# Performance work log

Hardware: AMD Instinct MI355X
Metric: run time of the kernel (lower is better)

## Reference

```python
import jax, jax.numpy as jnp
import numpy as np

N_NODES = 100000
N_EDGES = 1600000
D_IN = 128
D_OUT = 128
KEEP_PROB = 0.5  # torch code: p_drop = 1 - self.dropout, dropout=0.5


def setup_inputs() -> dict:
    key = jax.random.key(0)
    k1, k2, k3, k4, k5 = jax.random.split(key, 5)
    x = jax.random.normal(k1, (N_NODES, D_IN), dtype=jnp.float32)
    # Glorot uniform init matching weight_variable_glorot
    init_range = np.sqrt(6.0 / (D_IN + D_OUT))
    W = jax.random.uniform(k2, (D_IN, D_OUT), dtype=jnp.float32,
                           minval=-init_range, maxval=init_range)
    adj_row = jax.random.randint(k3, (N_EDGES,), 0, N_NODES, dtype=jnp.int32)
    adj_col = jax.random.randint(k4, (N_EDGES,), 0, N_NODES, dtype=jnp.int32)
    adj_val = jax.random.uniform(k5, (N_EDGES,), dtype=jnp.float32)
    return {"x": x, "W": W, "adj_row": adj_row, "adj_col": adj_col, "adj_val": adj_val}


def reference(x, W, adj_row, adj_col, adj_val):
    # dropout (always training=True in the torch module), deterministic key
    mask = jax.random.bernoulli(jax.random.key(42), KEEP_PROB, x.shape)
    x = jnp.where(mask, x / KEEP_PROB, 0.0)
    # dense GEMM: [N, D_in] @ [D_in, D_out]
    h = x @ W
    # sparse adjacency SpMM in COO form: out[r] += val * h[c]
    msg = adj_val[:, None] * h[adj_col]            # [E, D_out]
    agg = jax.ops.segment_sum(msg, adj_row, num_segments=N_NODES)
    return jax.nn.relu(agg)
```

## Files before the change

### kernel.cpp

```cpp
#include <hip/hip_runtime.h>
#include <hip/hip_bf16.h>

#define N_NODES 100000
#define N_EDGES 1600000
#define D 128
#define NC 391
#define CCAP 5120
#define C1S 32
#define RSS 257
#define G2CAP 512

typedef float          floatx4 __attribute__((ext_vector_type(4)));
typedef __bf16         bf16x8  __attribute__((ext_vector_type(8)));
typedef unsigned short ushort8 __attribute__((ext_vector_type(8)));

__device__ __forceinline__ unsigned rotl32(unsigned x, int d) {
    return (x << d) | (x >> (32 - d));
}

__device__ __forceinline__ void threefry_0_42(unsigned c0, unsigned c1,
                                              unsigned& o0, unsigned& o1) {
    const unsigned k0 = 0u, k1 = 42u;
    const unsigned k2 = 0x1BD11BDAu ^ k0 ^ k1;
    unsigned x0 = c0 + k0;
    unsigned x1 = c1 + k1;
#define TF_R4(r0, r1, r2, r3)                      \
    x0 += x1; x1 = rotl32(x1, r0); x1 ^= x0;       \
    x0 += x1; x1 = rotl32(x1, r1); x1 ^= x0;       \
    x0 += x1; x1 = rotl32(x1, r2); x1 ^= x0;       \
    x0 += x1; x1 = rotl32(x1, r3); x1 ^= x0;
    TF_R4(13, 15, 26, 6);  x0 += k1; x1 += k2 + 1u;
    TF_R4(17, 29, 16, 24); x0 += k2; x1 += k0 + 2u;
    TF_R4(13, 15, 26, 6);  x0 += k0; x1 += k1 + 3u;
    TF_R4(17, 29, 16, 24); x0 += k1; x1 += k2 + 4u;
    TF_R4(13, 15, 26, 6);  x0 += k2; x1 += k0 + 5u;
#undef TF_R4
    o0 = x0; o1 = x1;
}

__device__ __forceinline__ bool keep_elem(unsigned i) {
    unsigned o0, o1;
    threefry_0_42(0u, i, o0, o1);
    return (((o0 ^ o1) >> 31) == 0u);
}

__device__ __forceinline__ unsigned short f32_bf16(float f) {
    unsigned u = __float_as_uint(f);
    u += 0x7fffu + ((u >> 16) & 1u);
    return (unsigned short)(u >> 16);
}

__global__ __launch_bounds__(256)
void k_wprep(const float* __restrict__ W, unsigned short* __restrict__ Wf,
             int* __restrict__ cnt1) {
    int g = blockIdx.x * 256 + threadIdx.x;
    for (int i = g; i < NC * C1S; i += 2048) cnt1[i] = 0;
    int combo = g >> 6, l = g & 63;
    int ct = combo >> 2, kt = combo & 3;
    int mm = l & 15, q = l >> 4;
    unsigned short tmp[8];
#pragma unroll
    for (int j = 0; j < 8; ++j)
        tmp[j] = f32_bf16(W[(kt * 32 + q * 8 + j) * 128 + ct * 16 + mm]);
    *(ushort8*)&Wf[g * 8] = *(ushort8*)tmp;
}

__global__ __launch_bounds__(256)
void k_bucket1(const int* __restrict__ row, const int* __restrict__ col,
               const float* __restrict__ val, int* __restrict__ cnt1,
               int2* __restrict__ buf) {
    __shared__ int h[NC];
    __shared__ int lbase[NC];
    const int t = threadIdx.x;
    for (int i = t; i < NC; i += 256) h[i] = 0;
    __syncthreads();

    int rows[16], cols[16];
    float vals[16];
    int base = blockIdx.x * 4096;
#pragma unroll
    for (int k = 0; k < 4; ++k) {
        int e4 = base + (k * 256 + t) * 4;
        if (e4 < N_EDGES) {
            *(int4*)&rows[k * 4]   = *(const int4*)(row + e4);
            *(int4*)&cols[k * 4]   = *(const int4*)(col + e4);
            *(float4*)&vals[k * 4] = *(const float4*)(val + e4);
        } else {
            rows[k * 4] = rows[k * 4 + 1] = rows[k * 4 + 2] = rows[k * 4 + 3] = -1;
        }
    }
#pragma unroll
    for (int j = 0; j < 16; ++j)
        if (rows[j] >= 0) atomicAdd(&h[rows[j] >> 8], 1);
    __syncthreads();

    for (int i = t; i < NC; i += 256) {
        int c = h[i];
        lbase[i] = c ? atomicAdd(&cnt1[i * C1S], c) : 0;
    }
    __syncthreads();
    for (int i = t; i < NC; i += 256) h[i] = 0;
    __syncthreads();

#pragma unroll
    for (int j = 0; j < 16; ++j) {
        if (rows[j] >= 0) {
            int bb  = rows[j] >> 8;
            int pos = lbase[bb] + atomicAdd(&h[bb], 1);
            if (pos < CCAP) {
                int2 ent;
                ent.x = (cols[j] << 7) | ((rows[j] & 255) << 24);
                ent.y = __float_as_int(vals[j]);
                buf[bb * CCAP + pos] = ent;
            }
        }
    }
}

__global__ __launch_bounds__(256)
void k_sort(const int* __restrict__ cnt1, int2* __restrict__ buf,
            int* __restrict__ rs) {
    __shared__ int h[4][256];
    __shared__ int wsum[4];

    const int t = threadIdx.x;
    const int c = blockIdx.x;
    const int w = t >> 6;
    int n = cnt1[c * C1S];
    if (n > CCAP) n = CCAP;
    int2* slab = buf + c * CCAP;

    for (int i = t; i < 1024; i += 256) ((int*)h)[i] = 0;
    __syncthreads();

    int2 er[20];
#pragma unroll
    for (int k = 0; k < 20; ++k) {
        int i = k * 256 + t;
        if (i < n) {
            er[k] = slab[i];
            atomicAdd(&h[w][((unsigned)er[k].x) >> 24], 1);
        }
    }
    __syncthreads();

    int v = h[0][t] + h[1][t] + h[2][t] + h[3][t];
    int xsc = v;
#pragma unroll
    for (int off = 1; off < 64; off <<= 1) {
        int u = __shfl_up(xsc, off);
        if ((t & 63) >= off) xsc += u;
    }
    if ((t & 63) == 63) wsum[t >> 6] = xsc;
    __syncthreads();
    int wo = 0;
    for (int k = 0; k < (t >> 6); ++k) wo += wsum[k];
    int basex = xsc - v + wo;
    rs[c * RSS + t] = basex;
    if (t == 0) rs[c * RSS + 256] = n;
    int s = basex;
#pragma unroll
    for (int wv = 0; wv < 4; ++wv) {
        int tmp = h[wv][t];
        h[wv][t] = s;
        s += tmp;
    }
    __syncthreads();

#pragma unroll
    for (int k = 0; k < 20; ++k) {
        int i = k * 256 + t;
        if (i < n) {
            int pos = atomicAdd(&h[w][((unsigned)er[k].x) >> 24], 1);
            slab[pos] = er[k];
        }
    }
}

__global__ __launch_bounds__(256)
void k_gemm(const float* __restrict__ x, const unsigned short* __restrict__ Wf,
            unsigned short* __restrict__ hb) {
    __shared__ __align__(16) unsigned short xs[32][136];
    const int t = threadIdx.x, g = blockIdx.x;

    {
        int m  = t >> 4;
        int c0 = (t & 15) * 8;
        int r0 = g * 32 + m;
        const float* pa = x + r0 * D + c0;
        const float* pb = x + (r0 + 16) * D + c0;
        float va[8], vb[8];
        *(float4*)&va[0] = ((const float4*)pa)[0];
        *(float4*)&va[4] = ((const float4*)pa)[1];
        *(float4*)&vb[0] = ((const float4*)pb)[0];
        *(float4*)&vb[4] = ((const float4*)pb)[1];
        int ibase = r0 * D + c0;
        unsigned short ta[8], tb[8];
#pragma unroll
        for (int j = 0; j < 8; ++j) {
            float fa = keep_elem((unsigned)(ibase + j))        ? 2.0f * va[j] : 0.0f;
            float fb = keep_elem((unsigned)(ibase + 2048 + j)) ? 2.0f * vb[j] : 0.0f;
            ta[j] = f32_bf16(fa);
            tb[j] = f32_bf16(fb);
        }
        *(ushort8*)&xs[m][c0]      = *(ushort8*)ta;
        *(ushort8*)&xs[16 + m][c0] = *(ushort8*)tb;
    }
    __syncthreads();

    const int w = t >> 6, l = t & 63;
    const int rt = w >> 1, ctbase = (w & 1) * 4;
    const int mm = l & 15, q = l >> 4, koff = q * 8;
    const unsigned short* xrow = &xs[rt * 16 + mm][0];
    bf16x8 af[4];
#pragma unroll
    for (int kt = 0; kt < 4; ++kt)
        af[kt] = *(const bf16x8*)(xrow + kt * 32 + koff);

    const int growbase = g * 32 + rt * 16;
#pragma unroll
    for (int ci = 0; ci < 4; ++ci) {
        int ct = ctbase + ci;
        bf16x8 wfc[4];
#pragma unroll
        for (int kt = 0; kt < 4; ++kt)
            wfc[kt] = *(const bf16x8*)&Wf[((ct * 4 + kt) * 64 + l) * 8];
        floatx4 acc = {0.f, 0.f, 0.f, 0.f};
#pragma unroll
        for (int kt = 0; kt < 4; ++kt)
            acc = __builtin_amdgcn_mfma_f32_16x16x32_bf16(af[kt], wfc[kt], acc, 0, 0, 0);
        int col = ct * 16 + mm;
#pragma unroll
        for (int reg = 0; reg < 4; ++reg) {
            int grow = growbase + q * 4 + reg;
            hb[grow * D + col] = f32_bf16(acc[reg]);
        }
    }
}

__global__ __launch_bounds__(256, 8)
void k_gather(const int* __restrict__ rs, const int2* __restrict__ buf,
              const unsigned short* __restrict__ hb, float* __restrict__ out) {
    __shared__ __align__(16) int2 eL[G2CAP];

    const int B = blockIdx.x, t = threadIdx.x;
    const int c = B >> 4;
    const int2* slab = buf + c * CCAP;
    const int* rsb = rs + c * RSS + (B & 15) * 16;
    const int rs0 = rsb[0];
    int nf = rsb[16] - rs0;
    if (nf > G2CAP) nf = G2CAP;

    for (int i = t; i < nf; i += 256) eL[i] = slab[rs0 + i];
    __syncthreads();

    const int w  = t >> 6;
    const int l2 = (t & 63) * 2;
    const unsigned short* hbl = hb + l2;
    for (int r = 0; r < 4; ++r) {
        int rl = w * 4 + r;
        int s0 = rsb[rl] - rs0;     if (s0 > nf) s0 = nf;
        int e0 = rsb[rl + 1] - rs0; if (e0 > nf) e0 = nf;
        int cc = e0 - s0;
        float a0 = 0.f, a1 = 0.f;
        int i = 0;
        for (; i + 16 <= cc; i += 16) {
            unsigned ex[16];
            float    vv[16];
#pragma unroll
            for (int j = 0; j < 16; ++j) {
                int2 e = eL[s0 + i + j];
                ex[j] = (unsigned)e.x & 0xFFFFFFu;
                vv[j] = __int_as_float(e.y);
            }
            unsigned hv[16];
#pragma unroll
            for (int j = 0; j < 16; ++j)
                hv[j] = *(const unsigned*)(hbl + ex[j]);
#pragma unroll
            for (int j = 0; j < 16; ++j) {
                a0 = fmaf(vv[j], __uint_as_float(hv[j] << 16), a0);
                a1 = fmaf(vv[j], __uint_as_float(hv[j] & 0xffff0000u), a1);
            }
        }
        for (; i + 4 <= cc; i += 4) {
            unsigned ex[4];
            float    vv[4];
#pragma unroll
            for (int j = 0; j < 4; ++j) {
                int2 e = eL[s0 + i + j];
                ex[j] = (unsigned)e.x & 0xFFFFFFu;
                vv[j] = __int_as_float(e.y);
            }
            unsigned hv[4];
#pragma unroll
            for (int j = 0; j < 4; ++j)
                hv[j] = *(const unsigned*)(hbl + ex[j]);
#pragma unroll
            for (int j = 0; j < 4; ++j) {
                a0 = fmaf(vv[j], __uint_as_float(hv[j] << 16), a0);
                a1 = fmaf(vv[j], __uint_as_float(hv[j] & 0xffff0000u), a1);
            }
        }
        for (; i < cc; ++i) {
            int2 e = eL[s0 + i];
            float v = __int_as_float(e.y);
            unsigned hv = *(const unsigned*)(hbl + ((unsigned)e.x & 0xFFFFFFu));
            a0 = fmaf(v, __uint_as_float(hv << 16), a0);
            a1 = fmaf(v, __uint_as_float(hv & 0xffff0000u), a1);
        }
        int grow = (B << 4) + rl;
        if (grow < N_NODES) {
            float2 rr;
            rr.x = a0 > 0.f ? a0 : 0.f;
            rr.y = a1 > 0.f ? a1 : 0.f;
            *(float2*)(out + grow * D + l2) = rr;
        }
    }
}

extern "C" void kernel_launch(void* const* d_in, const int* in_sizes, int n_in,
                              void* d_out, int out_size, void* d_ws, size_t ws_size,
                              hipStream_t stream) {
    const float* x    = (const float*)d_in[0];
    const float* W    = (const float*)d_in[1];
    const int*   arow = (const int*)d_in[2];
    const int*   acol = (const int*)d_in[3];
    const float* aval = (const float*)d_in[4];
    float* out = (float*)d_out;

    char* ws = (char*)d_ws;
    unsigned short* hb = (unsigned short*)ws;
    size_t off = 25600000;
    int* cnt1 = (int*)(ws + off); off += NC * C1S * 4;
    off = (off + 127) & ~(size_t)127;
    unsigned short* Wf = (unsigned short*)(ws + off); off += 32768;
    off = (off + 127) & ~(size_t)127;
    int* rs   = (int*)(ws + off); off += NC * RSS * 4;
    off = (off + 127) & ~(size_t)127;
    int2* buf = (int2*)(ws + off); off += (size_t)NC * CCAP * 8;

    k_wprep   <<<8, 256, 0, stream>>>(W, Wf, cnt1);
    k_bucket1 <<<NC, 256, 0, stream>>>(arow, acol, aval, cnt1, buf);
    k_sort    <<<NC, 256, 0, stream>>>(cnt1, buf, rs);
    k_gemm    <<<3125, 256, 0, stream>>>(x, Wf, hb);
    k_gather  <<<NC * 16, 256, 0, stream>>>(rs, buf, hb, out);
}
```

Baseline: 227.2 us.

## Widen bucketing grid, double sort block size, stage GEMM output through LDS

The bucketing kernel now handles 1024 edges per block across 1563 blocks instead of 4096 per block across 391, which spreads the scatter over more CUs. The sort kernel runs 512 threads with 8 per-wave histograms. Only the first 256 threads do the scan, and a split __syncthreads handles the branch. The GEMM epilogue writes bf16 results into the shared tile and then stores full 16-byte rows, replacing scattered 2-byte global writes. The trade-offs are more global atomics on cnt1 and the shared-buffer reuse, plus the divergent-barrier pattern in the sort.

```diff
diff --git a/kernel.cpp b/kernel.cpp
--- a/kernel.cpp
+++ b/kernel.cpp
@@ -9,6 +9,7 @@
 #define C1S 32
 #define RSS 257
 #define G2CAP 512
+#define NB1 1563
 
 typedef float          floatx4 __attribute__((ext_vector_type(4)));
 typedef __bf16         bf16x8  __attribute__((ext_vector_type(8)));
@@ -75,22 +76,18 @@
     for (int i = t; i < NC; i += 256) h[i] = 0;
     __syncthreads();
 
-    int rows[16], cols[16];
-    float vals[16];
-    int base = blockIdx.x * 4096;
-#pragma unroll
-    for (int k = 0; k < 4; ++k) {
-        int e4 = base + (k * 256 + t) * 4;
-        if (e4 < N_EDGES) {
-            *(int4*)&rows[k * 4]   = *(const int4*)(row + e4);
-            *(int4*)&cols[k * 4]   = *(const int4*)(col + e4);
-            *(float4*)&vals[k * 4] = *(const float4*)(val + e4);
-        } else {
-            rows[k * 4] = rows[k * 4 + 1] = rows[k * 4 + 2] = rows[k * 4 + 3] = -1;
-        }
-    }
-#pragma unroll
-    for (int j = 0; j < 16; ++j)
+    int rows[4], cols[4];
+    float vals[4];
+    int e4 = blockIdx.x * 1024 + t * 4;
+    if (e4 < N_EDGES) {
+        *(int4*)&rows[0]   = *(const int4*)(row + e4);
+        *(int4*)&cols[0]   = *(const int4*)(col + e4);
+        *(float4*)&vals[0] = *(const float4*)(val + e4);
+    } else {
+        rows[0] = rows[1] = rows[2] = rows[3] = -1;
+    }
+#pragma unroll
+    for (int j = 0; j < 4; ++j)
         if (rows[j] >= 0) atomicAdd(&h[rows[j] >> 8], 1);
     __syncthreads();
 
@@ -103,7 +100,7 @@
     __syncthreads();
 
 #pragma unroll
-    for (int j = 0; j < 16; ++j) {
+    for (int j = 0; j < 4; ++j) {
         if (rows[j] >= 0) {
             int bb  = rows[j] >> 8;
             int pos = lbase[bb] + atomicAdd(&h[bb], 1);
@@ -117,10 +114,10 @@
     }
 }
 
-__global__ __launch_bounds__(256)
+__global__ __launch_bounds__(512)
 void k_sort(const int* __restrict__ cnt1, int2* __restrict__ buf,
             int* __restrict__ rs) {
-    __shared__ int h[4][256];
+    __shared__ int h[8][256];
     __shared__ int wsum[4];
 
     const int t = threadIdx.x;
@@ -130,13 +127,13 @@
     if (n > CCAP) n = CCAP;
     int2* slab = buf + c * CCAP;
 
-    for (int i = t; i < 1024; i += 256) ((int*)h)[i] = 0;
-    __syncthreads();
-
-    int2 er[20];
-#pragma unroll
-    for (int k = 0; k < 20; ++k) {
-        int i = k * 256 + t;
+    for (int i = t; i < 2048; i += 512) ((int*)h)[i] = 0;
+    __syncthreads();
+
+    int2 er[10];
+#pragma unroll
+    for (int k = 0; k < 10; ++k) {
+        int i = k * 512 + t;
         if (i < n) {
             er[k] = slab[i];
             atomicAdd(&h[w][((unsigned)er[k].x) >> 24], 1);
@@ -144,32 +141,38 @@
     }
     __syncthreads();
 
-    int v = h[0][t] + h[1][t] + h[2][t] + h[3][t];
-    int xsc = v;
-#pragma unroll
-    for (int off = 1; off < 64; off <<= 1) {
-        int u = __shfl_up(xsc, off);
-        if ((t & 63) >= off) xsc += u;
-    }
-    if ((t & 63) == 63) wsum[t >> 6] = xsc;
-    __syncthreads();
-    int wo = 0;
-    for (int k = 0; k < (t >> 6); ++k) wo += wsum[k];
-    int basex = xsc - v + wo;
-    rs[c * RSS + t] = basex;
-    if (t == 0) rs[c * RSS + 256] = n;
-    int s = basex;
-#pragma unroll
-    for (int wv = 0; wv < 4; ++wv) {
-        int tmp = h[wv][t];
-        h[wv][t] = s;
-        s += tmp;
-    }
-    __syncthreads();
-
-#pragma unroll
-    for (int k = 0; k < 20; ++k) {
-        int i = k * 256 + t;
+    if (t < 256) {
+        int v = 0;
+#pragma unroll
+        for (int wv = 0; wv < 8; ++wv) v += h[wv][t];
+        int xsc = v;
+#pragma unroll
+        for (int off = 1; off < 64; off <<= 1) {
+            int u = __shfl_up(xsc, off);
+            if ((t & 63) >= off) xsc += u;
+        }
+        if ((t & 63) == 63) wsum[t >> 6] = xsc;
+        __syncthreads();
+        int wo = 0;
+        for (int k = 0; k < (t >> 6); ++k) wo += wsum[k];
+        int basex = xsc - v + wo;
+        rs[c * RSS + t] = basex;
+        if (t == 0) rs[c * RSS + 256] = n;
+        int s = basex;
+#pragma unroll
+        for (int wv = 0; wv < 8; ++wv) {
+            int tmp = h[wv][t];
+            h[wv][t] = s;
+            s += tmp;
+        }
+    } else {
+        __syncthreads();
+    }
+    __syncthreads();
+
+#pragma unroll
+    for (int k = 0; k < 10; ++k) {
+        int i = k * 512 + t;
         if (i < n) {
             int pos = atomicAdd(&h[w][((unsigned)er[k].x) >> 24], 1);
             slab[pos] = er[k];
@@ -183,9 +186,10 @@
     __shared__ __align__(16) unsigned short xs[32][136];
     const int t = threadIdx.x, g = blockIdx.x;
 
+    const int m  = t >> 4;
+    const int c0 = (t & 15) * 8;
+
     {
-        int m  = t >> 4;
-        int c0 = (t & 15) * 8;
         int r0 = g * 32 + m;
         const float* pa = x + r0 * D + c0;
         const float* pb = x + (r0 + 16) * D + c0;
@@ -217,7 +221,7 @@
     for (int kt = 0; kt < 4; ++kt)
         af[kt] = *(const bf16x8*)(xrow + kt * 32 + koff);
 
-    const int growbase = g * 32 + rt * 16;
+    floatx4 accs[4];
 #pragma unroll
     for (int ci = 0; ci < 4; ++ci) {
         int ct = ctbase + ci;
@@ -229,12 +233,22 @@
 #pragma unroll
         for (int kt = 0; kt < 4; ++kt)
             acc = __builtin_amdgcn_mfma_f32_16x16x32_bf16(af[kt], wfc[kt], acc, 0, 0, 0);
-        int col = ct * 16 + mm;
-#pragma unroll
-        for (int reg = 0; reg < 4; ++reg) {
-            int grow = growbase + q * 4 + reg;
-            hb[grow * D + col] = f32_bf16(acc[reg]);
-        }
+        accs[ci] = acc;
+    }
+
+    __syncthreads();
+#pragma unroll
+    for (int ci = 0; ci < 4; ++ci) {
+        int col = (ctbase + ci) * 16 + mm;
+#pragma unroll
+        for (int reg = 0; reg < 4; ++reg)
+            xs[rt * 16 + q * 4 + reg][col] = f32_bf16(accs[ci][reg]);
+    }
+    __syncthreads();
+    {
+        int r0 = g * 32 + m;
+        *(ushort8*)&hb[r0 * D + c0]        = *(ushort8*)&xs[m][c0];
+        *(ushort8*)&hb[(r0 + 16) * D + c0] = *(ushort8*)&xs[16 + m][c0];
     }
 }
 
@@ -341,8 +355,8 @@
     int2* buf = (int2*)(ws + off); off += (size_t)NC * CCAP * 8;
 
     k_wprep   <<<8, 256, 0, stream>>>(W, Wf, cnt1);
-    k_bucket1 <<<NC, 256, 0, stream>>>(arow, acol, aval, cnt1, buf);
-    k_sort    <<<NC, 256, 0, stream>>>(cnt1, buf, rs);
+    k_bucket1 <<<NB1, 256, 0, stream>>>(arow, acol, aval, cnt1, buf);
+    k_sort    <<<NC, 512, 0, stream>>>(cnt1, buf, rs);
     k_gemm    <<<3125, 256, 0, stream>>>(x, Wf, hb);
     k_gather  <<<NC * 16, 256, 0, stream>>>(rs, buf, hb, out);
 }
```

Measured after the change: 251.0 us. 1.1x slower.
